# Kernel optimization log

Measured on AMD Instinct MI355X. Metric: run time of the kernel, lower is better.

## Reference

```python
import jax, jax.numpy as jnp
from jax import lax
import numpy as np

B, N = 8, 16384
C = 16            # layer_channels
K = 2             # kernel_size
L = 30            # layer_nums (layer 0 is plain causal conv, 29 gated layers)
AGG = 64          # agregate1x1 out channels
OUT = 256         # output1x1 out channels (8-bit classes)


def causal_conv(x, w, dilation):
    # x: (B, Cin, N), w: (Cout, Cin, K) -> (B, Cout, N), left-padded (causal)
    k = w.shape[-1]
    return lax.conv_general_dilated(
        x, w, window_strides=(1,), padding=[(dilation * (k - 1), 0)],
        rhs_dilation=(dilation,), dimension_numbers=('NCH', 'OIH', 'NCH'))


def setup_inputs() -> dict:
    key = jax.random.key(0)
    ks = jax.random.split(key, 16)
    s = 0.1
    x = jax.random.normal(ks[0], (B, N), dtype=jnp.float32) * 8000.0  # raw 16-bit-ish audio
    lengths = jax.random.randint(ks[1], (B,), N // 2, N, dtype=jnp.int32)
    return {
        'x': x,
        'lengths': lengths,
        'W0': jax.random.normal(ks[2], (C, 1, K), dtype=jnp.float32) * s,
        'b0': jnp.zeros((C,), dtype=jnp.float32),
        'Wf': jax.random.normal(ks[3], (L - 1, C, C, K), dtype=jnp.float32) * s,
        'bf': jnp.zeros((L - 1, C), dtype=jnp.float32),
        'Wg': jax.random.normal(ks[4], (L - 1, C, C, K), dtype=jnp.float32) * s,
        'bg': jnp.zeros((L - 1, C), dtype=jnp.float32),
        'Wr': jax.random.normal(ks[5], (L - 1, C, C), dtype=jnp.float32) * s,
        'br': jnp.zeros((L - 1, C), dtype=jnp.float32),
        'Wa': jax.random.normal(ks[6], (AGG, C), dtype=jnp.float32) * s,
        'ba': jnp.zeros((AGG,), dtype=jnp.float32),
        'Wo': jax.random.normal(ks[7], (OUT, AGG), dtype=jnp.float32) * s,
        'bo': jnp.zeros((OUT,), dtype=jnp.float32),
    }


def reference(x, lengths, W0, b0, Wf, bf, Wg, bg, Wr, br, Wa, ba, Wo, bo):
    inp = (x / 32768.0)[:, None, :]                     # (B,1,N), 65536/2 scaling
    # layer 0: plain causal conv 1 -> C
    h = causal_conv(inp, W0, 1) + b0[:, None]           # (B,C,N)
    skip = h
    inp = inp + h                                       # (B,1,N)+(B,C,N) broadcast
    for i in range(1, L):
        d = 2 ** (i % 10)
        j = i - 1
        f = jnp.tanh(causal_conv(inp, Wf[j], d) + bf[j][:, None])
        g = jax.nn.sigmoid(causal_conv(inp, Wg[j], d) + bg[j][:, None])
        z = f * g                                       # gated activation
        out = jnp.einsum('oc,bcn->bon', Wr[j], z) + br[j][:, None]
        skip = skip + out                               # skip-sum accumulation
        inp = inp + out                                 # residual
    a = jnp.einsum('oc,bcn->bon', Wa, jax.nn.relu(skip)) + ba[:, None]
    o = jnp.einsum('oc,bcn->bon', Wo, jax.nn.relu(a)) + bo[:, None]
    logp = jax.nn.log_softmax(o, axis=1)                # (B,OUT,N)
    mask = (jnp.arange(N) < lengths[:, None])[:, None, :].astype(logp.dtype)
    return logp * mask
```

## Files before the change

### kernel.cpp

```cpp
#include <hip/hip_runtime.h>
#include <hip/hip_bf16.h>

#define NN 16384
#define NC 16
#define NPOSTOT 131072
#define NLAY 29
#define TOUT 256
#define LSTR 24

typedef float4 f4;
typedef short bf16x8 __attribute__((ext_vector_type(8)));
typedef float f32x4 __attribute__((ext_vector_type(4)));

#define OFF_WF 0
#define OFF_WG (NLAY * 512)
#define OFF_WR (2 * NLAY * 512)
#define OFF_WA (3 * NLAY * 512)
#define OFF_WO (3 * NLAY * 512 + 2048)
#define PK_TOT (OFF_WO + 16384)

static __device__ __forceinline__ short to_bf16(float f) {
    __hip_bfloat16 h = __float2bfloat16(f);
    short s;
    __builtin_memcpy(&s, &h, 2);
    return s;
}
static __device__ __forceinline__ float from_bf16(short s) {
    unsigned int u = ((unsigned int)(unsigned short)s) << 16;
    float f;
    __builtin_memcpy(&f, &u, 4);
    return f;
}

__global__ __launch_bounds__(256) void prepack_k(
    const float* __restrict__ Wf, const float* __restrict__ Wg,
    const float* __restrict__ Wr, const float* __restrict__ Wa,
    const float* __restrict__ Wo, short* __restrict__ pk)
{
    const int i = blockIdx.x * 256 + threadIdx.x;
    if (i >= PK_TOT) return;
    float val;
    if (i < OFF_WG) {
        const int j = i >> 9, r = i & 511, l = r >> 3, j8 = r & 7;
        const int o = l & 15, h = l >> 4;
        const int k = h * 8 + j8, tap = k >> 4, c = k & 15;
        val = Wf[((j * 16 + o) * 16 + c) * 2 + tap];
    } else if (i < OFF_WA) {
        const int i2 = i - OFF_WG;
        if (i2 < NLAY * 512) {
            const int j = i2 >> 9, r = i2 & 511, l = r >> 3, j8 = r & 7;
            const int o = l & 15, h = l >> 4;
            const int k = h * 8 + j8, tap = k >> 4, c = k & 15;
            val = Wg[((j * 16 + o) * 16 + c) * 2 + tap];
        } else {
            const int i3 = i2 - NLAY * 512;
            const int j = i3 >> 9, r = i3 & 511, l = r >> 3, j8 = r & 7;
            const int o = l & 15, h = l >> 4;
            val = (j8 < 4) ? Wr[j * 256 + o * 16 + h * 4 + j8] : 0.0f;
        }
    } else if (i < OFF_WO) {
        const int i2 = i - OFF_WA;
        const int mt = i2 >> 9, r = i2 & 511, l = r >> 3, j8 = r & 7;
        const int og = mt * 16 + (l & 15), h = l >> 4;
        const int k = h * 8 + j8;
        val = (k < 16) ? Wa[og * 16 + k] : 0.0f;
    } else {
        const int i2 = i - OFF_WO;
        const int qt = i2 >> 10, hf = (i2 >> 9) & 1, r = i2 & 511;
        const int l = r >> 3, j8 = r & 7;
        const int q = qt * 16 + (l & 15), h = l >> 4;
        const int kg = hf * 32 + (j8 >> 2) * 16 + h * 4 + (j8 & 3);
        val = Wo[q * 64 + kg];
    }
    pk[i] = to_bf16(val);
}

static __device__ __forceinline__ f32x4 gated_core2(
    bf16x8 bx, bf16x8 af_, bf16x8 ag_, bf16x8 ar_,
    f32x4 cf, f32x4 cg, f32x4 cr)
{
    const f32x4 fp = __builtin_amdgcn_mfma_f32_16x16x32_bf16(af_, bx, cf, 0, 0, 0);
    const f32x4 gp = __builtin_amdgcn_mfma_f32_16x16x32_bf16(ag_, bx, cg, 0, 0, 0);

    bf16x8 bz;
#pragma unroll
    for (int r = 0; r < 4; ++r) {
        const float ef = __expf(2.0f * fminf(fp[r], 43.0f));
        const float eg = __expf(-gp[r]);
        const float den = fmaf(ef, eg, ef) + (eg + 1.0f);
        bz[r] = to_bf16((ef - 1.0f) * __builtin_amdgcn_rcpf(den));
        bz[r + 4] = 0;
    }
    return __builtin_amdgcn_mfma_f32_16x16x32_bf16(ar_, bz, cr, 0, 0, 0);
}

struct SegCfg { int d[8]; int nl; int jbase; int H; int l0; };

constexpr SegCfg CFGS[6] = {
    {{2, 4, 8, 16, 32, 64, 0, 0},     6, 0,  128, 1},
    {{128, 256, 0, 0, 0, 0, 0, 0},    2, 6,  256, 0},
    {{512, 1, 2, 4, 8, 16, 32, 64},   8, 8,  128, 0},
    {{128, 256, 0, 0, 0, 0, 0, 0},    2, 16, 256, 0},
    {{512, 1, 2, 4, 8, 16, 32, 64},   8, 18, 128, 0},
    {{128, 256, 0, 0, 0, 0, 0, 0},    2, 26, 256, 0},
};

template<int KI>
__global__ __launch_bounds__((TOUT + CFGS[KI].H) * 2)
void fused_t(const short* __restrict__ src, const float* __restrict__ x,
             const float* __restrict__ W0, const float* __restrict__ b0,
             short* __restrict__ dst, const short* __restrict__ pk,
             const float* __restrict__ bfA, const float* __restrict__ bgA,
             const float* __restrict__ brA)
{
    constexpr SegCfg cfg = CFGS[KI];
    constexpr int H = cfg.H;
    constexpr int Wp = TOUT + H;
    constexpr bool MULTI = (cfg.nl > 1);
    constexpr int LDSSZ = MULTI ? 2 * Wp * LSTR : 8;
    __shared__ short lds[LDSSZ];
    short* ldsA = lds;
    short* ldsB = lds + (MULTI ? Wp * LSTR : 0);

    const int t = threadIdx.x, lane = t & 63, wv = t >> 6;
    const int h = lane >> 4, i16 = lane & 15;
    const int tap = h >> 1, c0 = (h & 1) * 8;
    const int pbase = blockIdx.x * TOUT;
    const int bb = pbase >> 14, n0 = pbase & (NN - 1);
    const float* xrow = x + (size_t)bb * NN;
    const short* srow = src + (size_t)bb * NN * NC;

    const int l0r = wv * 32 + i16;
    const int l1r = l0r + 16;
    const int nA = n0 - H + l0r;
    const int nB = nA + 16;

    f32x4 res0, res1;

    {
        constexpr int d = cfg.d[0];
        constexpr int j = cfg.jbase;
        const bf16x8 af = *(const bf16x8*)(pk + OFF_WF + j * 512 + lane * 8);
        const bf16x8 ag = *(const bf16x8*)(pk + OFF_WG + j * 512 + lane * 8);
        const bf16x8 ar = *(const bf16x8*)(pk + OFF_WR + j * 512 + lane * 8);
        const f4 v1 = *(const f4*)(bfA + j * 16 + h * 4);
        const f4 v2 = *(const f4*)(bgA + j * 16 + h * 4);
        const f4 v3 = *(const f4*)(brA + j * 16 + h * 4);
        const f32x4 cf = {v1.x, v1.y, v1.z, v1.w};
        const f32x4 cg = {v2.x, v2.y, v2.z, v2.w};
        const f32x4 cr = {v3.x, v3.y, v3.z, v3.w};

        auto tile0 = [&](int l, int n, f32x4& res) {
            const int ns = tap ? n : n - d;
            bf16x8 bx = {0, 0, 0, 0, 0, 0, 0, 0};
            if (cfg.l0) {
                if (ns >= 0) {
                    const float xs = xrow[ns] * (1.0f / 32768.0f);
                    const float xm = (ns >= 1) ? xrow[ns - 1] * (1.0f / 32768.0f) : 0.0f;
#pragma unroll
                    for (int q2 = 0; q2 < 8; ++q2) {
                        const int c = c0 + q2;
                        bx[q2] = to_bf16(xs + fmaf(W0[c * 2], xm,
                                          fmaf(W0[c * 2 + 1], xs, b0[c])));
                    }
                }
            } else {
                if (ns >= 0) bx = *(const bf16x8*)(srow + (size_t)ns * NC + c0);
            }
            const f32x4 o = gated_core2(bx, af, ag, ar, cf, cg, cr);

            float r0, r1, r2, r3;
            if (cfg.l0) {
                if (n >= 0) {
                    const float xs = xrow[n] * (1.0f / 32768.0f);
                    const float xm = (n >= 1) ? xrow[n - 1] * (1.0f / 32768.0f) : 0.0f;
                    const int c = h * 4;
                    r0 = xs + fmaf(W0[c * 2 + 0], xm, fmaf(W0[c * 2 + 1], xs, b0[c + 0]));
                    r1 = xs + fmaf(W0[c * 2 + 2], xm, fmaf(W0[c * 2 + 3], xs, b0[c + 1]));
                    r2 = xs + fmaf(W0[c * 2 + 4], xm, fmaf(W0[c * 2 + 5], xs, b0[c + 2]));
                    r3 = xs + fmaf(W0[c * 2 + 6], xm, fmaf(W0[c * 2 + 7], xs, b0[c + 3]));
                } else { r0 = r1 = r2 = r3 = 0.0f; }
            } else {
                if (n >= 0) {
                    const short4 ov = *(const short4*)(srow + (size_t)n * NC + h * 4);
                    r0 = from_bf16(ov.x); r1 = from_bf16(ov.y);
                    r2 = from_bf16(ov.z); r3 = from_bf16(ov.w);
                } else { r0 = r1 = r2 = r3 = 0.0f; }
            }
            res[0] = r0 + o[0]; res[1] = r1 + o[1];
            res[2] = r2 + o[2]; res[3] = r3 + o[3];
            if (MULTI) {
                *(short4*)(ldsA + l * LSTR + h * 4) =
                    make_short4(to_bf16(res[0]), to_bf16(res[1]),
                                to_bf16(res[2]), to_bf16(res[3]));
            }
        };
        tile0(l0r, nA, res0);
        tile0(l1r, nB, res1);
    }
    if (MULTI) __syncthreads();

    int cur = 0;
#pragma unroll
    for (int s = 1; s < cfg.nl; ++s) {
        const int d = cfg.d[s];
        const int j = cfg.jbase + s;
        const bf16x8 af = *(const bf16x8*)(pk + OFF_WF + j * 512 + lane * 8);
        const bf16x8 ag = *(const bf16x8*)(pk + OFF_WG + j * 512 + lane * 8);
        const bf16x8 ar = *(const bf16x8*)(pk + OFF_WR + j * 512 + lane * 8);
        const f4 v1 = *(const f4*)(bfA + j * 16 + h * 4);
        const f4 v2 = *(const f4*)(bgA + j * 16 + h * 4);
        const f4 v3 = *(const f4*)(brA + j * 16 + h * 4);
        const f32x4 cf = {v1.x, v1.y, v1.z, v1.w};
        const f32x4 cg = {v2.x, v2.y, v2.z, v2.w};
        const f32x4 cr = {v3.x, v3.y, v3.z, v3.w};
        const short* rb = cur ? ldsB : ldsA;
        short* wb = cur ? ldsA : ldsB;
        const bool wr = (s + 1 < cfg.nl);

        auto tileL = [&](int l, int n, f32x4& res) {
            const int nt = tap ? n : n - d;
            int lt = tap ? l : l - d;
            if (lt < 0) lt = 0;
            bf16x8 bx = {0, 0, 0, 0, 0, 0, 0, 0};
            if (nt >= 0) bx = *(const bf16x8*)(rb + lt * LSTR + c0);
            const f32x4 o = gated_core2(bx, af, ag, ar, cf, cg, cr);
            res[0] += o[0]; res[1] += o[1]; res[2] += o[2]; res[3] += o[3];
            if (wr) {
                *(short4*)(wb + l * LSTR + h * 4) =
                    make_short4(to_bf16(res[0]), to_bf16(res[1]),
                                to_bf16(res[2]), to_bf16(res[3]));
            }
        };
        tileL(l0r, nA, res0);
        tileL(l1r, nB, res1);
        if (s + 1 < cfg.nl) __syncthreads();
        cur ^= 1;
    }

    if (l0r >= H) {
        *(short4*)(dst + ((size_t)bb * NN + nA) * NC + h * 4) =
            make_short4(to_bf16(res0[0]), to_bf16(res0[1]),
                        to_bf16(res0[2]), to_bf16(res0[3]));
    }
    if (l1r >= H) {
        *(short4*)(dst + ((size_t)bb * NN + nB) * NC + h * 4) =
            make_short4(to_bf16(res1[0]), to_bf16(res1[1]),
                        to_bf16(res1[2]), to_bf16(res1[3]));
    }
}

__global__ __launch_bounds__(512, 2) void headm_k(
    const short* __restrict__ src, const float* __restrict__ x,
    const int* __restrict__ lengths, const short* __restrict__ pk,
    const float* __restrict__ bfL, const float* __restrict__ bgL,
    const float* __restrict__ brL,
    const short* __restrict__ pka, const float* __restrict__ ba,
    const short* __restrict__ pko, const float* __restrict__ bo,
    float* __restrict__ out)
{
    __shared__ short ldsW[16384];
    __shared__ short ldsS[8][256];

    const int t = threadIdx.x;
    const int lane = t & 63;
    const int wv = t >> 6;
    const int i16 = lane & 15;
    const int h = lane >> 4;
    const int pos = blockIdx.x * 128 + wv * 16 + i16;
    const int b = pos >> 14;
    const int n = pos & (NN - 1);

#pragma unroll
    for (int i = 0; i < 4; ++i)
        ((f4*)ldsW)[t + i * 512] = ((const f4*)pko)[t + i * 512];

    {
        constexpr int j = NLAY - 1;
        constexpr int d = 512;
        const short* srow = src + (size_t)b * NN * NC;
        const int tap = h >> 1, c0 = (h & 1) * 8;
        const int ns = tap ? n : n - d;
        bf16x8 bx = {0, 0, 0, 0, 0, 0, 0, 0};
        if (ns >= 0) bx = *(const bf16x8*)(srow + (size_t)ns * NC + c0);

        const bf16x8 af = *(const bf16x8*)(pk + OFF_WF + j * 512 + lane * 8);
        const bf16x8 ag = *(const bf16x8*)(pk + OFF_WG + j * 512 + lane * 8);
        const bf16x8 ar = *(const bf16x8*)(pk + OFF_WR + j * 512 + lane * 8);
        const f4 v1 = *(const f4*)(bfL + j * 16 + h * 4);
        const f4 v2 = *(const f4*)(bgL + j * 16 + h * 4);
        const f4 v3 = *(const f4*)(brL + j * 16 + h * 4);
        const f32x4 cf = {v1.x, v1.y, v1.z, v1.w};
        const f32x4 cg = {v2.x, v2.y, v2.z, v2.w};
        const f32x4 cr = {v3.x, v3.y, v3.z, v3.w};
        const f32x4 o = gated_core2(bx, af, ag, ar, cf, cg, cr);

        const short4 ov = *(const short4*)(srow + (size_t)n * NC + h * 4);
        const float xs = x[pos] * (1.0f / 32768.0f);
        const short4 w = make_short4(
            to_bf16(fmaxf(from_bf16(ov.x) + o[0] - xs, 0.0f)),
            to_bf16(fmaxf(from_bf16(ov.y) + o[1] - xs, 0.0f)),
            to_bf16(fmaxf(from_bf16(ov.z) + o[2] - xs, 0.0f)),
            to_bf16(fmaxf(from_bf16(ov.w) + o[3] - xs, 0.0f)));
        *(short4*)(&ldsS[wv][i16 * 16 + h * 4]) = w;
    }
    __syncthreads();

    bf16x8 bs;
    if (h < 2) {
        bs = *(const bf16x8*)(&ldsS[wv][i16 * 16 + h * 8]);
    } else {
#pragma unroll
        for (int j = 0; j < 8; ++j) bs[j] = 0;
    }

    float ra[16];
#pragma unroll
    for (int mt = 0; mt < 4; ++mt) {
        const bf16x8 aa = *(const bf16x8*)(pka + (mt * 64 + lane) * 8);
        const f4 bav = *(const f4*)(ba + mt * 16 + h * 4);
        f32x4 c = {bav.x, bav.y, bav.z, bav.w};
        c = __builtin_amdgcn_mfma_f32_16x16x32_bf16(aa, bs, c, 0, 0, 0);
#pragma unroll
        for (int r = 0; r < 4; ++r) ra[mt * 4 + r] = fmaxf(c[r], 0.0f);
    }
    bf16x8 blo, bhi;
#pragma unroll
    for (int j = 0; j < 8; ++j) { blo[j] = to_bf16(ra[j]); bhi[j] = to_bf16(ra[8 + j]); }

    float lg[64];
#pragma unroll
    for (int qt = 0; qt < 16; ++qt) {
        const bf16x8 a0 = *(const bf16x8*)(ldsW + ((qt * 2 + 0) * 64 + lane) * 8);
        const bf16x8 a1 = *(const bf16x8*)(ldsW + ((qt * 2 + 1) * 64 + lane) * 8);
        const f4 bov = *(const f4*)(bo + qt * 16 + h * 4);
        f32x4 c = {bov.x, bov.y, bov.z, bov.w};
        c = __builtin_amdgcn_mfma_f32_16x16x32_bf16(a0, blo, c, 0, 0, 0);
        c = __builtin_amdgcn_mfma_f32_16x16x32_bf16(a1, bhi, c, 0, 0, 0);
#pragma unroll
        for (int r = 0; r < 4; ++r) lg[qt * 4 + r] = c[r];
    }

    float m = lg[0];
#pragma unroll
    for (int j = 1; j < 64; ++j) m = fmaxf(m, lg[j]);
    m = fmaxf(m, __shfl_xor(m, 16, 64));
    m = fmaxf(m, __shfl_xor(m, 32, 64));
    float s = 0.0f;
#pragma unroll
    for (int j = 0; j < 64; ++j) s += __expf(lg[j] - m);
    s += __shfl_xor(s, 16, 64);
    s += __shfl_xor(s, 32, 64);
    const float lse = m + __logf(s);
    const bool valid = n < lengths[b];

    float* ob = out + (size_t)b * 256 * NN + n;
#pragma unroll
    for (int qt = 0; qt < 16; ++qt)
#pragma unroll
        for (int r = 0; r < 4; ++r)
            ob[(size_t)(qt * 16 + h * 4 + r) * NN] = valid ? (lg[qt * 4 + r] - lse) : 0.0f;
}

extern "C" void kernel_launch(void* const* d_in, const int* in_sizes, int n_in,
                              void* d_out, int out_size, void* d_ws, size_t ws_size,
                              hipStream_t stream)
{
    const float* x       = (const float*)d_in[0];
    const int*   lengths = (const int*)d_in[1];
    const float* W0      = (const float*)d_in[2];
    const float* b0      = (const float*)d_in[3];
    const float* Wf      = (const float*)d_in[4];
    const float* bf      = (const float*)d_in[5];
    const float* Wg      = (const float*)d_in[6];
    const float* bg      = (const float*)d_in[7];
    const float* Wr      = (const float*)d_in[8];
    const float* br      = (const float*)d_in[9];
    const float* Wa      = (const float*)d_in[10];
    const float* ba      = (const float*)d_in[11];
    const float* Wo      = (const float*)d_in[12];
    const float* bo      = (const float*)d_in[13];
    float* out = (float*)d_out;

    short* bufA = (short*)d_ws;
    short* bufB = bufA + (size_t)NPOSTOT * NC;
    short* pk   = bufB + (size_t)NPOSTOT * NC;

    prepack_k<<<dim3((PK_TOT + 255) / 256), dim3(256), 0, stream>>>(
        Wf, Wg, Wr, Wa, Wo, pk);

#define FUSED(K, SRC, DST)                                                     \
    fused_t<K><<<dim3(NPOSTOT / TOUT), dim3((TOUT + CFGS[K].H) * 2), 0,        \
                 stream>>>(SRC, x, W0, b0, DST, pk, bf, bg, br)

    FUSED(0, bufA, bufA);
    FUSED(1, bufA, bufB);
    FUSED(2, bufB, bufA);
    FUSED(3, bufA, bufB);
    FUSED(4, bufB, bufA);
    FUSED(5, bufA, bufB);
#undef FUSED

    headm_k<<<dim3(NPOSTOT / 128), dim3(512), 0, stream>>>(
        bufB, x, lengths, pk, bf, bg, br,
        pk + OFF_WA, ba, pk + OFF_WO, bo, out);
}
```

Baseline: 136.2 us.

## Fold layer 27 into head kernel, recomputing its dilated tap in-block

The last segment kernel now runs only layer 26 (dilation 128). The head kernel computes layer 27 (dilation 256) itself, at both n and n-512, so layer 28's dilation-512 taps come from LDS and not from a global intermediate. This removes one global write and read pass of the residual, and the dependent layer 27 output buffer. The price is doubled layer 27 compute and extra source loads inside the head kernel. The __syncthreads is also moved later, after the aggregate matmul.

```diff
diff --git a/kernel.cpp b/kernel.cpp
--- a/kernel.cpp
+++ b/kernel.cpp
@@ -102,7 +102,7 @@
     {{512, 1, 2, 4, 8, 16, 32, 64},   8, 8,  128, 0},
     {{128, 256, 0, 0, 0, 0, 0, 0},    2, 16, 256, 0},
     {{512, 1, 2, 4, 8, 16, 32, 64},   8, 18, 128, 0},
-    {{128, 256, 0, 0, 0, 0, 0, 0},    2, 26, 256, 0},
+    {{128, 0, 0, 0, 0, 0, 0, 0},      1, 26, 0,   0},
 };
 
 template<int KI>
@@ -260,7 +260,9 @@
     float* __restrict__ out)
 {
     __shared__ short ldsW[16384];
-    __shared__ short ldsS[8][256];
+    __shared__ short ldsS0[8][256];
+    __shared__ short ldsS1[8][256];
+    __shared__ short ldsS2[8][256];
 
     const int t = threadIdx.x;
     const int lane = t & 63;
@@ -270,20 +272,16 @@
     const int pos = blockIdx.x * 128 + wv * 16 + i16;
     const int b = pos >> 14;
     const int n = pos & (NN - 1);
+    const int tap = h >> 1, c0 = (h & 1) * 8;
+    const short* srow = src + (size_t)b * NN * NC;
 
 #pragma unroll
     for (int i = 0; i < 4; ++i)
         ((f4*)ldsW)[t + i * 512] = ((const f4*)pko)[t + i * 512];
 
+    f32x4 r27n;
     {
-        constexpr int j = NLAY - 1;
-        constexpr int d = 512;
-        const short* srow = src + (size_t)b * NN * NC;
-        const int tap = h >> 1, c0 = (h & 1) * 8;
-        const int ns = tap ? n : n - d;
-        bf16x8 bx = {0, 0, 0, 0, 0, 0, 0, 0};
-        if (ns >= 0) bx = *(const bf16x8*)(srow + (size_t)ns * NC + c0);
-
+        constexpr int j = NLAY - 2;
         const bf16x8 af = *(const bf16x8*)(pk + OFF_WF + j * 512 + lane * 8);
         const bf16x8 ag = *(const bf16x8*)(pk + OFF_WG + j * 512 + lane * 8);
         const bf16x8 ar = *(const bf16x8*)(pk + OFF_WR + j * 512 + lane * 8);
@@ -293,22 +291,56 @@
         const f32x4 cf = {v1.x, v1.y, v1.z, v1.w};
         const f32x4 cg = {v2.x, v2.y, v2.z, v2.w};
         const f32x4 cr = {v3.x, v3.y, v3.z, v3.w};
+
+        auto run27 = [&](int p, short* dstS) -> f32x4 {
+            const int ns = tap ? p : p - 256;
+            bf16x8 bx = {0, 0, 0, 0, 0, 0, 0, 0};
+            if (ns >= 0) bx = *(const bf16x8*)(srow + (size_t)ns * NC + c0);
+            const f32x4 o = gated_core2(bx, af, ag, ar, cf, cg, cr);
+            const short4 ov = *(const short4*)(srow + (size_t)p * NC + h * 4);
+            f32x4 r;
+            r[0] = from_bf16(ov.x) + o[0]; r[1] = from_bf16(ov.y) + o[1];
+            r[2] = from_bf16(ov.z) + o[2]; r[3] = from_bf16(ov.w) + o[3];
+            *(short4*)(dstS + i16 * 16 + h * 4) =
+                make_short4(to_bf16(r[0]), to_bf16(r[1]),
+                            to_bf16(r[2]), to_bf16(r[3]));
+            return r;
+        };
+        r27n = run27(n, &ldsS0[wv][0]);
+        if (n >= 512) run27(n - 512, &ldsS1[wv][0]);
+    }
+
+    {
+        constexpr int j = NLAY - 1;
+        const bf16x8 af = *(const bf16x8*)(pk + OFF_WF + j * 512 + lane * 8);
+        const bf16x8 ag = *(const bf16x8*)(pk + OFF_WG + j * 512 + lane * 8);
+        const bf16x8 ar = *(const bf16x8*)(pk + OFF_WR + j * 512 + lane * 8);
+        const f4 v1 = *(const f4*)(bfL + j * 16 + h * 4);
+        const f4 v2 = *(const f4*)(bgL + j * 16 + h * 4);
+        const f4 v3 = *(const f4*)(brL + j * 16 + h * 4);
+        const f32x4 cf = {v1.x, v1.y, v1.z, v1.w};
+        const f32x4 cg = {v2.x, v2.y, v2.z, v2.w};
+        const f32x4 cr = {v3.x, v3.y, v3.z, v3.w};
+
+        bf16x8 bx = {0, 0, 0, 0, 0, 0, 0, 0};
+        if (tap) {
+            bx = *(const bf16x8*)(&ldsS0[wv][i16 * 16 + c0]);
+        } else if (n >= 512) {
+            bx = *(const bf16x8*)(&ldsS1[wv][i16 * 16 + c0]);
+        }
         const f32x4 o = gated_core2(bx, af, ag, ar, cf, cg, cr);
 
-        const short4 ov = *(const short4*)(srow + (size_t)n * NC + h * 4);
         const float xs = x[pos] * (1.0f / 32768.0f);
-        const short4 w = make_short4(
-            to_bf16(fmaxf(from_bf16(ov.x) + o[0] - xs, 0.0f)),
-            to_bf16(fmaxf(from_bf16(ov.y) + o[1] - xs, 0.0f)),
-            to_bf16(fmaxf(from_bf16(ov.z) + o[2] - xs, 0.0f)),
-            to_bf16(fmaxf(from_bf16(ov.w) + o[3] - xs, 0.0f)));
-        *(short4*)(&ldsS[wv][i16 * 16 + h * 4]) = w;
-    }
-    __syncthreads();
+        *(short4*)(&ldsS2[wv][i16 * 16 + h * 4]) = make_short4(
+            to_bf16(fmaxf(r27n[0] + o[0] - xs, 0.0f)),
+            to_bf16(fmaxf(r27n[1] + o[1] - xs, 0.0f)),
+            to_bf16(fmaxf(r27n[2] + o[2] - xs, 0.0f)),
+            to_bf16(fmaxf(r27n[3] + o[3] - xs, 0.0f)));
+    }
 
     bf16x8 bs;
     if (h < 2) {
-        bs = *(const bf16x8*)(&ldsS[wv][i16 * 16 + h * 8]);
+        bs = *(const bf16x8*)(&ldsS2[wv][i16 * 16 + h * 8]);
     } else {
 #pragma unroll
         for (int j = 0; j < 8; ++j) bs[j] = 0;
@@ -327,6 +359,8 @@
     bf16x8 blo, bhi;
 #pragma unroll
     for (int j = 0; j < 8; ++j) { blo[j] = to_bf16(ra[j]); bhi[j] = to_bf16(ra[8 + j]); }
+
+    __syncthreads();
 
     float lg[64];
 #pragma unroll
```

Measured after the change: 132.4 us. 2.7% less time.
